# Kernel optimization log

Measured on AMD Instinct MI355X. Metric: run time of the kernel, lower is better.

Reference implementation:

```python
import jax, jax.numpy as jnp
import numpy as np


def setup_inputs() -> dict:
    key = jax.random.key(0)
    ks = jax.random.split(key, 8)
    B, L, D = 8, 4096, 1024
    s = 1.0 / np.sqrt(D)  # torch Linear default init scale (approx)
    return {
        "x": jax.random.normal(ks[0], (B, L, D), dtype=jnp.float32),
        "hidden": jax.random.normal(ks[1], (B, D), dtype=jnp.float32),
        "W_f": jax.random.normal(ks[2], (D, D), dtype=jnp.float32) * s,
        "b_f": jnp.zeros((D,), dtype=jnp.float32),
        "W_i": jax.random.normal(ks[3], (D, D), dtype=jnp.float32) * s,
        "b_i": jnp.zeros((D,), dtype=jnp.float32),
        "W_o": jax.random.normal(ks[4], (D, D), dtype=jnp.float32) * s,
        "b_o": jnp.zeros((D,), dtype=jnp.float32),
    }


def reference(x, hidden, W_f, b_f, W_i, b_i, W_o, b_o):
    # x: [B, L, D], hidden: [B, D]
    D = x.shape[-1]
    lin = jnp.linspace(0.0, 1.0, D, dtype=x.dtype)  # per-channel gate scale
    remember = jax.nn.sigmoid(jnp.einsum('bld,ed->ble', x, W_f) + b_f) * lin
    forget = 1.0 - remember
    inp = jnp.tanh(jnp.einsum('bld,ed->ble', x, W_i) + b_i) * remember

    # linear recurrence h_t = forget_t * h_{t-1} + inp_t  via parallel scan
    def combine(c1, c2):
        a1, u1 = c1
        a2, u2 = c2
        return (a1 * a2, a2 * u1 + u2)

    cumprod_forget, h_inner = jax.lax.associative_scan(combine, (forget, inp), axis=1)
    h = h_inner + hidden[:, None, :] * cumprod_forget  # inject initial hidden state
    y = jnp.einsum('bld,ed->ble', h, W_o) + b_o
    return y, h
```

## Files before the change

kernel.cpp:

```cpp
#include <hip/hip_runtime.h>
#include <stdint.h>

#define B_ 8
#define L_ 4096
#define D_ 1024
#define M_ (B_*L_)
#define CHUNKS 128
#define TCH (L_/CHUNKS)

typedef float f32x4 __attribute__((ext_vector_type(4)));
typedef float f32x2 __attribute__((ext_vector_type(2)));
typedef short short8 __attribute__((ext_vector_type(8)));
typedef unsigned short ushort4v __attribute__((ext_vector_type(4)));

static __device__ __forceinline__ unsigned short f2bf(float f) {
  union { float f; unsigned u; } v; v.f = f;
  unsigned r = v.u + 0x7FFFu + ((v.u >> 16) & 1u);
  return (unsigned short)(r >> 16);
}
static __device__ __forceinline__ float bf2f(unsigned short u) {
  union { unsigned u; float f; } v; v.u = ((unsigned)u) << 16; return v.f;
}

#define GLOAD16(g, l) \
  __builtin_amdgcn_global_load_lds((__attribute__((address_space(1))) const void*)(g), \
                                   (__attribute__((address_space(3))) void*)(l), 16, 0, 0)

__global__ __launch_bounds__(256)
void cvt_bf16(const float* __restrict__ src, unsigned short* __restrict__ dst, int n8)
{
  int gid = blockIdx.x * 256 + threadIdx.x;
  if (gid >= n8) return;
  const f32x4* s = (const f32x4*)(src + (size_t)gid * 8);
  f32x4 v0 = s[0], v1 = s[1];
  union { short8 v; unsigned short u[8]; } w;
  w.u[0] = f2bf(v0[0]); w.u[1] = f2bf(v0[1]); w.u[2] = f2bf(v0[2]); w.u[3] = f2bf(v0[3]);
  w.u[4] = f2bf(v1[0]); w.u[5] = f2bf(v1[1]); w.u[6] = f2bf(v1[2]); w.u[7] = f2bf(v1[3]);
  *(short8*)(dst + (size_t)gid * 8) = w.v;
}

__global__ __launch_bounds__(256)
void cvt_w3(const float* __restrict__ w0, const float* __restrict__ w1,
            const float* __restrict__ w2, unsigned short* __restrict__ dst)
{
  const int per = (D_ * D_) / 8 / 256;
  int m = blockIdx.x / per;
  int gid = (blockIdx.x % per) * 256 + threadIdx.x;
  const float* src = (m == 0) ? w0 : (m == 1) ? w1 : w2;
  const f32x4* s = (const f32x4*)(src + (size_t)gid * 8);
  f32x4 v0 = s[0], v1 = s[1];
  union { short8 v; unsigned short u[8]; } w;
  w.u[0] = f2bf(v0[0]); w.u[1] = f2bf(v0[1]); w.u[2] = f2bf(v0[2]); w.u[3] = f2bf(v0[3]);
  w.u[4] = f2bf(v1[0]); w.u[5] = f2bf(v1[1]); w.u[6] = f2bf(v1[2]); w.u[7] = f2bf(v1[3]);
  *(short8*)(dst + (size_t)m * D_ * D_ + (size_t)gid * 8) = w.v;
}

template<int MODE>
__global__ __launch_bounds__(512, 2)
void gemm256(const unsigned short* __restrict__ A,
             const unsigned short* __restrict__ Bw,
             const float* __restrict__ bias0,
             const float* __restrict__ bias1,
             unsigned short* __restrict__ ob0,
             unsigned short* __restrict__ ob1,
             float* __restrict__ of)
{
  __shared__ unsigned short lds[65536];
  char* ldsb = (char*)lds;

  const int tid  = threadIdx.x;
  const int lane = tid & 63;
  const int wid  = tid >> 6;
  const int wm   = wid >> 2;
  const int wn   = wid & 3;
  const int frow = lane & 15, ks = lane >> 4;
  const int xsw  = (ks ^ ((frow >> 1) & 3)) << 4;

  constexpr int NBN = (MODE == 0) ? 8 : 4;
  constexpr int GBM = 32 / NBN;
  const int xcd   = blockIdx.x & 7;
  const int slot  = blockIdx.x >> 3;
  const int local = slot & 31;
  const int wrnd  = slot >> 5;
  const int bm = (xcd * 16 + wrnd * GBM + (local & (GBM - 1))) * 256;
  const int bn = (local / GBM) * 256;

  const int r0  = tid >> 2;
  const int scl = ((tid & 3) ^ ((r0 >> 1) & 3)) << 4;
  const char* pA = (const char*)A  + (size_t)(bm + r0) * 2048 + scl;
  const char* pB = (const char*)Bw + (size_t)(bn + r0) * 2048 + scl;
  const int dst16 = tid * 16;

  f32x4 acc[8][4] = {};
  short8 aq[4], bq[4];

  auto stgA = [&](int T, int kk, int buf) {
    const char* s = pA + T * 128 + kk * 64;
    char* d = ldsb + buf * 32768 + kk * 16384 + dst16;
    GLOAD16(s, d);
    GLOAD16(s + (size_t)128 * 2048, d + 8192);
  };
  auto stgB = [&](int T, int kk, int buf) {
    const char* s = pB + T * 128 + kk * 64;
    char* d = ldsb + 65536 + buf * 32768 + kk * 16384 + dst16;
    GLOAD16(s, d);
    GLOAD16(s + (size_t)128 * 2048, d + 8192);
  };
  auto ldAB4 = [&](const char* LA, const char* LB, int kk, int ih) {
    const char* ab = LA + kk * 16384 + (wm * 128 + ih * 64 + frow) * 64 + xsw;
    const char* bb = LB + kk * 16384 + (wn * 64 + frow) * 64 + xsw;
    aq[0] = *(const short8*)(ab);
    bq[0] = *(const short8*)(bb);
    bq[1] = *(const short8*)(bb + 1024);
    bq[2] = *(const short8*)(bb + 2048);
    bq[3] = *(const short8*)(bb + 3072);
    aq[1] = *(const short8*)(ab + 1024);
    aq[2] = *(const short8*)(ab + 2048);
    aq[3] = *(const short8*)(ab + 3072);
  };
  auto ldA4 = [&](const char* LA, int kk, int ih) {
    const char* ab = LA + kk * 16384 + (wm * 128 + ih * 64 + frow) * 64 + xsw;
    aq[0] = *(const short8*)(ab);
    aq[1] = *(const short8*)(ab + 1024);
    aq[2] = *(const short8*)(ab + 2048);
    aq[3] = *(const short8*)(ab + 3072);
  };
  auto mfma16 = [&](int ih) {
    __builtin_amdgcn_s_setprio(1);
    #pragma unroll
    for (int i2 = 0; i2 < 4; ++i2) {
      #pragma unroll
      for (int j = 0; j < 4; ++j)
        acc[ih * 4 + i2][j] =
          __builtin_amdgcn_mfma_f32_16x16x32_bf16(aq[i2], bq[j], acc[ih * 4 + i2][j], 0, 0, 0);
    }
    __builtin_amdgcn_s_setprio(0);
  };

#define DO_TILE(T, BUF, STG1, STG2, W1, W3)                                   \
  {                                                                           \
    const char* LA = ldsb + (BUF) * 32768;                                    \
    const char* LB = ldsb + 65536 + (BUF) * 32768;                            \
    ldAB4(LA, LB, 0, 0);                                                      \
    if (STG1) stgA((T) + 1, 1, ((T) + 1) & 1);                                \
    __builtin_amdgcn_s_barrier();                                             \
    mfma16(0);                                                                \
    __builtin_amdgcn_s_barrier();                                             \
    ldA4(LA, 0, 1);                                                           \
    if (STG1) stgB((T) + 1, 1, ((T) + 1) & 1);                                \
    asm volatile("s_waitcnt vmcnt(" #W1 ")" ::: "memory");                    \
    __builtin_amdgcn_s_barrier();                                             \
    mfma16(1);                                                                \
    __builtin_amdgcn_s_barrier();                                             \
    ldAB4(LA, LB, 1, 0);                                                      \
    if (STG2) stgA((T) + 2, 0, (BUF));                                        \
    __builtin_amdgcn_s_barrier();                                             \
    mfma16(0);                                                                \
    __builtin_amdgcn_s_barrier();                                             \
    ldA4(LA, 1, 1);                                                           \
    if (STG2) stgB((T) + 2, 0, (BUF));                                        \
    asm volatile("s_waitcnt vmcnt(" #W3 ")" ::: "memory");                    \
    __builtin_amdgcn_s_barrier();                                             \
    mfma16(1);                                                                \
    __builtin_amdgcn_s_barrier();                                             \
  }

  stgA(0, 0, 0); stgB(0, 0, 0);
  stgA(0, 1, 0); stgB(0, 1, 0);
  stgA(1, 0, 1); stgB(1, 0, 1);
  asm volatile("s_waitcnt vmcnt(8)" ::: "memory");
  __builtin_amdgcn_s_barrier();

  for (int tt = 0; tt < 7; ++tt) {
    int t0 = tt * 2;
    DO_TILE(t0,     0, true, true, 8, 8);
    DO_TILE(t0 + 1, 1, true, true, 8, 8);
  }
  DO_TILE(14, 0, true,  false, 8, 4);
  DO_TILE(15, 1, false, false, 0, 0);
#undef DO_TILE

  if constexpr (MODE == 0) {
    const int plane = bn >> 10;
    const int cb    = bn & 1023;
    unsigned short* ob = plane ? ob1 : ob0;
    const float* bs    = plane ? bias1 : bias0;
    float bv[4];
    #pragma unroll
    for (int j = 0; j < 4; ++j) bv[j] = bs[cb + wn * 64 + j * 16 + frow];
    #pragma unroll
    for (int ii = 0; ii < 8; ++ii) {
      int row = bm + wm * 128 + ii * 16 + ks * 4;
      #pragma unroll
      for (int j = 0; j < 4; ++j) {
        int col = cb + wn * 64 + j * 16 + frow;
        float lin = (float)col * (1.0f / 1023.0f);
        #pragma unroll
        for (int r = 0; r < 4; ++r) {
          float z = acc[ii][j][r] + bv[j];
          float v;
          if (plane == 0) {
            v = lin / (1.0f + __expf(-z));
          } else {
            float e2 = __expf(2.0f * z);
            v = 1.0f - 2.0f / (e2 + 1.0f);
          }
          ob[(size_t)(row + r) * D_ + col] = f2bf(v);
        }
      }
    }
  } else {
    float bv[4];
    #pragma unroll
    for (int j = 0; j < 4; ++j) bv[j] = bias0[bn + wn * 64 + j * 16 + frow];
    #pragma unroll
    for (int ii = 0; ii < 8; ++ii) {
      int row = bm + wm * 128 + ii * 16 + ks * 4;
      #pragma unroll
      for (int j = 0; j < 4; ++j) {
        int col = bn + wn * 64 + j * 16 + frow;
        #pragma unroll
        for (int r = 0; r < 4; ++r)
          of[(size_t)(row + r) * D_ + col] = acc[ii][j][r] + bv[j];
      }
    }
  }
}

__global__ __launch_bounds__(256)
void scan_partial_b(const unsigned short* __restrict__ rb,
                    const unsigned short* __restrict__ tb,
                    float* __restrict__ Ag, float* __restrict__ Ug)
{
  int blk = blockIdx.x;
  int b = blk >> 7, c = blk & (CHUNKS - 1);
  int e = threadIdx.x << 2;
  size_t base = ((size_t)b * L_ + (size_t)c * TCH) * D_ + e;
  f32x4 a = {1.f,1.f,1.f,1.f}, u = {0.f,0.f,0.f,0.f};
  for (int t = 0; t < TCH; ++t) {
    ushort4v r4 = *(const ushort4v*)(rb + base + (size_t)t * D_);
    ushort4v t4 = *(const ushort4v*)(tb + base + (size_t)t * D_);
    #pragma unroll
    for (int j = 0; j < 4; ++j) {
      float rem = bf2f(r4[j]);
      float f   = 1.0f - rem;
      float inp = bf2f(t4[j]) * rem;
      u[j] = fmaf(f, u[j], inp);
      a[j] *= f;
    }
  }
  size_t o = (size_t)(b * CHUNKS + c) * D_ + e;
  *(f32x4*)(Ag + o) = a;
  *(f32x4*)(Ug + o) = u;
}

__global__ __launch_bounds__(256)
void scan_carry(const float* __restrict__ Ag, const float* __restrict__ Ug,
                const float* __restrict__ hidden, float* __restrict__ Hin)
{
  int gid = blockIdx.x * 256 + threadIdx.x;
  int b = gid >> 8;
  int e = (gid & 255) << 2;
  f32x4 h = *(const f32x4*)(hidden + (size_t)b * D_ + e);
  for (int c = 0; c < CHUNKS; ++c) {
    size_t o = (size_t)(b * CHUNKS + c) * D_ + e;
    *(f32x4*)(Hin + o) = h;
    f32x4 A = *(const f32x4*)(Ag + o);
    f32x4 U = *(const f32x4*)(Ug + o);
    h = A * h + U;
  }
}

__global__ __launch_bounds__(256)
void scan_apply_b(const unsigned short* __restrict__ rb,
                  const unsigned short* __restrict__ tb,
                  const float* __restrict__ Hin,
                  float* __restrict__ hout, unsigned short* __restrict__ hb)
{
  int blk = blockIdx.x;
  int b = blk >> 7, c = blk & (CHUNKS - 1);
  int e = threadIdx.x << 2;
  size_t base = ((size_t)b * L_ + (size_t)c * TCH) * D_ + e;
  f32x4 h = *(const f32x4*)(Hin + (size_t)(b * CHUNKS + c) * D_ + e);
  for (int t = 0; t < TCH; ++t) {
    size_t o = base + (size_t)t * D_;
    ushort4v r4 = *(const ushort4v*)(rb + o);
    ushort4v t4 = *(const ushort4v*)(tb + o);
    #pragma unroll
    for (int j = 0; j < 4; ++j) {
      float rem = bf2f(r4[j]);
      float f   = 1.0f - rem;
      float inp = bf2f(t4[j]) * rem;
      h[j] = fmaf(f, h[j], inp);
    }
    *(f32x4*)(hout + o) = h;
    ushort4v p;
    p[0] = f2bf(h[0]); p[1] = f2bf(h[1]); p[2] = f2bf(h[2]); p[3] = f2bf(h[3]);
    *(ushort4v*)(hb + o) = p;
  }
}

template<int MODE>
__global__ __launch_bounds__(256, 2)
void gemm_slow(const float* __restrict__ A, const float* __restrict__ B0,
               const float* __restrict__ B1, const float* __restrict__ bias0,
               const float* __restrict__ bias1, float* __restrict__ out0,
               float* __restrict__ out1)
{
  constexpr int BK = 32;
  __shared__ unsigned short As[128 * BK];
  __shared__ unsigned short Bs0[128 * BK];
  __shared__ unsigned short Bs1[(MODE == 0) ? (128 * BK) : 8];

  const int tid = threadIdx.x, lane = tid & 63, wave = tid >> 6;
  const int wr = wave >> 1, wc = wave & 1;
  const int bm = blockIdx.x * 128, bn = blockIdx.y * 128;
  f32x4 acc0[4][4] = {};
  f32x4 acc1[(MODE == 0) ? 4 : 1][(MODE == 0) ? 4 : 1] = {};
  const int frow = lane & 15, kslot = lane >> 4;
  const int xs = kslot ^ (frow & 3);

  auto stage = [&](const float* src, unsigned short* dst) {
    #pragma unroll
    for (int p = 0; p < 4; ++p) {
      int g = p * 256 + tid;
      int row = g >> 3, kq = (g & 7) << 2;
      f32x4 v = *(const f32x4*)(src + (size_t)row * D_ + kq);
      ushort4v w;
      w[0] = f2bf(v[0]); w[1] = f2bf(v[1]); w[2] = f2bf(v[2]); w[3] = f2bf(v[3]);
      int byte = kq << 1, slot = byte >> 4, sub = byte & 15;
      int off = row * 64 + ((slot ^ (row & 3)) << 4) + sub;
      *(ushort4v*)((char*)dst + off) = w;
    }
  };

  for (int k0 = 0; k0 < D_; k0 += BK) {
    stage(A + (size_t)bm * D_ + k0, As);
    stage(B0 + (size_t)bn * D_ + k0, Bs0);
    if constexpr (MODE == 0) stage(B1 + (size_t)bn * D_ + k0, Bs1);
    __syncthreads();
    short8 af[4], bf0[4], bf1[4];
    #pragma unroll
    for (int i = 0; i < 4; ++i) {
      int ar = wr * 64 + i * 16 + frow;
      af[i] = *(const short8*)((const char*)As + ar * 64 + (xs << 4));
      int br = wc * 64 + i * 16 + frow;
      bf0[i] = *(const short8*)((const char*)Bs0 + br * 64 + (xs << 4));
      if constexpr (MODE == 0)
        bf1[i] = *(const short8*)((const char*)Bs1 + br * 64 + (xs << 4));
    }
    #pragma unroll
    for (int i = 0; i < 4; ++i)
      #pragma unroll
      for (int j = 0; j < 4; ++j) {
        acc0[i][j] = __builtin_amdgcn_mfma_f32_16x16x32_bf16(af[i], bf0[j], acc0[i][j], 0, 0, 0);
        if constexpr (MODE == 0)
          acc1[i][j] = __builtin_amdgcn_mfma_f32_16x16x32_bf16(af[i], bf1[j], acc1[i][j], 0, 0, 0);
      }
    __syncthreads();
  }
  #pragma unroll
  for (int i = 0; i < 4; ++i)
    #pragma unroll
    for (int j = 0; j < 4; ++j)
      #pragma unroll
      for (int r = 0; r < 4; ++r) {
        int row = bm + wr * 64 + i * 16 + (lane >> 4) * 4 + r;
        int col = bn + wc * 64 + j * 16 + (lane & 15);
        size_t idx = (size_t)row * D_ + col;
        if constexpr (MODE == 0) {
          float zf = acc0[i][j][r] + bias0[col];
          float linv = (float)col * (1.0f / 1023.0f);
          float rem = linv / (1.0f + __expf(-zf));
          float zi = acc1[i][j][r] + bias1[col];
          float e2 = __expf(2.0f * zi);
          float th = 1.0f - 2.0f / (e2 + 1.0f);
          out0[idx] = 1.0f - rem;
          out1[idx] = th * rem;
        } else {
          out0[idx] = acc0[i][j][r] + bias0[col];
        }
      }
}

__global__ __launch_bounds__(256)
void scan_partial_f(const float* __restrict__ p0, const float* __restrict__ p1,
                    float* __restrict__ Ag, float* __restrict__ Ug)
{
  int blk = blockIdx.x;
  int b = blk / (CHUNKS * 2);
  int c = (blk >> 1) & (CHUNKS - 1);
  int e = ((blk & 1) << 9) + threadIdx.x * 2;
  size_t base = ((size_t)b * L_ + (size_t)c * TCH) * D_ + e;
  f32x2 a = {1.0f, 1.0f}, u = {0.0f, 0.0f};
  for (int t = 0; t < TCH; ++t) {
    f32x2 f = *(const f32x2*)(p0 + base + (size_t)t * D_);
    f32x2 i = *(const f32x2*)(p1 + base + (size_t)t * D_);
    u = f * u + i;
    a = a * f;
  }
  size_t o = (size_t)(b * CHUNKS + c) * D_ + e;
  *(f32x2*)(Ag + o) = a;
  *(f32x2*)(Ug + o) = u;
}

__global__ __launch_bounds__(256)
void scan_apply_f(const float* __restrict__ p0, float* __restrict__ p1_io,
                  const float* __restrict__ Hin)
{
  int blk = blockIdx.x;
  int b = blk / (CHUNKS * 2);
  int c = (blk >> 1) & (CHUNKS - 1);
  int e = ((blk & 1) << 9) + threadIdx.x * 2;
  size_t base = ((size_t)b * L_ + (size_t)c * TCH) * D_ + e;
  f32x2 h = *(const f32x2*)(Hin + (size_t)(b * CHUNKS + c) * D_ + e);
  for (int t = 0; t < TCH; ++t) {
    size_t o = base + (size_t)t * D_;
    f32x2 f = *(const f32x2*)(p0 + o);
    f32x2 i = *(const f32x2*)(p1_io + o);
    h = f * h + i;
    *(f32x2*)(p1_io + o) = h;
  }
}

extern "C" void kernel_launch(void* const* d_in, const int* in_sizes, int n_in,
                              void* d_out, int out_size, void* d_ws, size_t ws_size,
                              hipStream_t stream)
{
  const float* x      = (const float*)d_in[0];
  const float* hidden = (const float*)d_in[1];
  const float* W_f    = (const float*)d_in[2];
  const float* b_f    = (const float*)d_in[3];
  const float* W_i    = (const float*)d_in[4];
  const float* b_i    = (const float*)d_in[5];
  const float* W_o    = (const float*)d_in[6];
  const float* b_o    = (const float*)d_in[7];

  float* y = (float*)d_out;
  float* h = y + (size_t)M_ * D_;

  const size_t xb_elems = (size_t)M_ * D_;
  const size_t w_elems  = (size_t)D_ * D_;
  const size_t agg      = (size_t)B_ * CHUNKS * D_;
  const size_t need = (xb_elems * 3 + 3 * w_elems) * 2 + agg * 3 * 4;

  if (ws_size >= need) {
    unsigned short* xb  = (unsigned short*)d_ws;
    unsigned short* wfb = xb + xb_elems;
    unsigned short* wib = wfb + w_elems;
    unsigned short* wob = wib + w_elems;
    unsigned short* rbv = wob + w_elems;
    unsigned short* tbv = rbv + xb_elems;
    float* Ag  = (float*)(tbv + xb_elems);
    float* Ug  = Ag + agg;
    float* Hin = Ug + agg;

    cvt_bf16<<<(int)(xb_elems / 8 / 256), 256, 0, stream>>>(x, xb, (int)(xb_elems / 8));
    cvt_w3<<<3 * (int)(w_elems / 8 / 256), 256, 0, stream>>>(W_f, W_i, W_o, wfb);

    gemm256<0><<<1024, 512, 0, stream>>>(xb, wfb, b_f, b_i, rbv, tbv, nullptr);

    int pblocks = B_ * CHUNKS;
    scan_partial_b<<<pblocks, 256, 0, stream>>>(rbv, tbv, Ag, Ug);
    scan_carry<<<(B_ * D_ / 4) / 256, 256, 0, stream>>>(Ag, Ug, hidden, Hin);
    scan_apply_b<<<pblocks, 256, 0, stream>>>(rbv, tbv, Hin, h, xb);

    gemm256<1><<<512, 512, 0, stream>>>(xb, wob, b_o, nullptr, nullptr, nullptr, y);
  } else {
    float* Ag  = (float*)d_ws;
    float* Ug  = Ag + agg;
    float* Hin = Ug + agg;
    dim3 gg(M_ / 128, D_ / 128);
    int pblocks = B_ * CHUNKS * 2;

    gemm_slow<0><<<gg, 256, 0, stream>>>(x, W_f, W_i, b_f, b_i, y, h);
    scan_partial_f<<<pblocks, 256, 0, stream>>>(y, h, Ag, Ug);
    scan_carry<<<(B_ * D_ / 4) / 256, 256, 0, stream>>>(Ag, Ug, hidden, Hin);
    scan_apply_f<<<pblocks, 256, 0, stream>>>(y, h, Hin);
    gemm_slow<1><<<gg, 256, 0, stream>>>(h, W_o, nullptr, b_o, nullptr, y, nullptr);
  }
}
```

Baseline: 388.7 us.

## Triple-buffer A tiles in LDS and restructure GEMM prefetch schedule

```diff
diff --git a/kernel.cpp b/kernel.cpp
--- a/kernel.cpp
+++ b/kernel.cpp
@@ -65,7 +65,7 @@
              unsigned short* __restrict__ ob1,
              float* __restrict__ of)
 {
-  __shared__ unsigned short lds[65536];
+  __shared__ unsigned short lds[81920];
   char* ldsb = (char*)lds;
 
   const int tid  = threadIdx.x;
@@ -94,20 +94,24 @@
   f32x4 acc[8][4] = {};
   short8 aq[4], bq[4];
 
-  auto stgA = [&](int T, int kk, int buf) {
-    const char* s = pA + T * 128 + kk * 64;
-    char* d = ldsb + buf * 32768 + kk * 16384 + dst16;
-    GLOAD16(s, d);
+  auto stgA = [&](int T, int sl) {
+    const char* s = pA + T * 128;
+    char* d = ldsb + sl * 32768 + dst16;
+    GLOAD16(s,                      d);
     GLOAD16(s + (size_t)128 * 2048, d + 8192);
-  };
-  auto stgB = [&](int T, int kk, int buf) {
-    const char* s = pB + T * 128 + kk * 64;
-    char* d = ldsb + 65536 + buf * 32768 + kk * 16384 + dst16;
-    GLOAD16(s, d);
+    GLOAD16(s + 64,                      d + 16384);
+    GLOAD16(s + 64 + (size_t)128 * 2048, d + 24576);
+  };
+  auto stgB = [&](int T, int sl) {
+    const char* s = pB + T * 128;
+    char* d = ldsb + 98304 + sl * 32768 + dst16;
+    GLOAD16(s,                      d);
     GLOAD16(s + (size_t)128 * 2048, d + 8192);
-  };
-  auto ldAB4 = [&](const char* LA, const char* LB, int kk, int ih) {
-    const char* ab = LA + kk * 16384 + (wm * 128 + ih * 64 + frow) * 64 + xsw;
+    GLOAD16(s + 64,                      d + 16384);
+    GLOAD16(s + 64 + (size_t)128 * 2048, d + 24576);
+  };
+  auto ldAB4 = [&](const char* LA, const char* LB, int kk) {
+    const char* ab = LA + kk * 16384 + (wm * 128 + frow) * 64 + xsw;
     const char* bb = LB + kk * 16384 + (wn * 64 + frow) * 64 + xsw;
     aq[0] = *(const short8*)(ab);
     bq[0] = *(const short8*)(bb);
@@ -118,8 +122,8 @@
     aq[2] = *(const short8*)(ab + 2048);
     aq[3] = *(const short8*)(ab + 3072);
   };
-  auto ldA4 = [&](const char* LA, int kk, int ih) {
-    const char* ab = LA + kk * 16384 + (wm * 128 + ih * 64 + frow) * 64 + xsw;
+  auto ldA4 = [&](const char* LA, int kk) {
+    const char* ab = LA + kk * 16384 + (wm * 128 + 64 + frow) * 64 + xsw;
     aq[0] = *(const short8*)(ab);
     aq[1] = *(const short8*)(ab + 1024);
     aq[2] = *(const short8*)(ab + 2048);
@@ -137,48 +141,51 @@
     __builtin_amdgcn_s_setprio(0);
   };
 
-#define DO_TILE(T, BUF, STG1, STG2, W1, W3)                                   \
+#define BAR __builtin_amdgcn_s_barrier()
+#define DO_TILE(T, SA, SB, SAst, SBst, STGB, STGA, WAITN)                     \
   {                                                                           \
-    const char* LA = ldsb + (BUF) * 32768;                                    \
-    const char* LB = ldsb + 65536 + (BUF) * 32768;                            \
-    ldAB4(LA, LB, 0, 0);                                                      \
-    if (STG1) stgA((T) + 1, 1, ((T) + 1) & 1);                                \
-    __builtin_amdgcn_s_barrier();                                             \
-    mfma16(0);                                                                \
-    __builtin_amdgcn_s_barrier();                                             \
-    ldA4(LA, 0, 1);                                                           \
-    if (STG1) stgB((T) + 1, 1, ((T) + 1) & 1);                                \
-    asm volatile("s_waitcnt vmcnt(" #W1 ")" ::: "memory");                    \
-    __builtin_amdgcn_s_barrier();                                             \
-    mfma16(1);                                                                \
-    __builtin_amdgcn_s_barrier();                                             \
-    ldAB4(LA, LB, 1, 0);                                                      \
-    if (STG2) stgA((T) + 2, 0, (BUF));                                        \
-    __builtin_amdgcn_s_barrier();                                             \
-    mfma16(0);                                                                \
-    __builtin_amdgcn_s_barrier();                                             \
-    ldA4(LA, 1, 1);                                                           \
-    if (STG2) stgB((T) + 2, 0, (BUF));                                        \
-    asm volatile("s_waitcnt vmcnt(" #W3 ")" ::: "memory");                    \
-    __builtin_amdgcn_s_barrier();                                             \
-    mfma16(1);                                                                \
-    __builtin_amdgcn_s_barrier();                                             \
-  }
-
-  stgA(0, 0, 0); stgB(0, 0, 0);
-  stgA(0, 1, 0); stgB(0, 1, 0);
-  stgA(1, 0, 1); stgB(1, 0, 1);
+    const char* LA = ldsb + (SA) * 32768;                                     \
+    const char* LB = ldsb + 98304 + (SB) * 32768;                             \
+    ldAB4(LA, LB, 0);                                                         \
+    if (STGB) stgB((T) + 1, (SBst));                                          \
+    if (STGA) stgA((T) + 2, (SAst));                                          \
+    BAR; mfma16(0); BAR;                                                      \
+    ldA4(LA, 0);                                                              \
+    BAR; mfma16(1); BAR;                                                      \
+    ldAB4(LA, LB, 1);                                                         \
+    BAR; mfma16(0); BAR;                                                      \
+    ldA4(LA, 1);                                                              \
+    BAR; mfma16(1);                                                           \
+    if ((WAITN) >= 0) {                                                       \
+      if ((WAITN) == 4) asm volatile("s_waitcnt vmcnt(4)" ::: "memory");      \
+      else              asm volatile("s_waitcnt vmcnt(0)" ::: "memory");      \
+    }                                                                         \
+    BAR;                                                                      \
+  }
+
+  stgB(0, 0); stgA(0, 0);
+  stgB(1, 1); stgA(1, 1);
   asm volatile("s_waitcnt vmcnt(8)" ::: "memory");
-  __builtin_amdgcn_s_barrier();
-
-  for (int tt = 0; tt < 7; ++tt) {
-    int t0 = tt * 2;
-    DO_TILE(t0,     0, true, true, 8, 8);
-    DO_TILE(t0 + 1, 1, true, true, 8, 8);
-  }
-  DO_TILE(14, 0, true,  false, 8, 4);
-  DO_TILE(15, 1, false, false, 0, 0);
+  BAR;
+
+  DO_TILE( 0, 0, 0, 2, 1, false, true,  4);
+  DO_TILE( 1, 1, 1, 0, 0, true,  true,  4);
+  DO_TILE( 2, 2, 0, 1, 1, true,  true,  4);
+  DO_TILE( 3, 0, 1, 2, 0, true,  true,  4);
+  DO_TILE( 4, 1, 0, 0, 1, true,  true,  4);
+  DO_TILE( 5, 2, 1, 1, 0, true,  true,  4);
+  DO_TILE( 6, 0, 0, 2, 1, true,  true,  4);
+  DO_TILE( 7, 1, 1, 0, 0, true,  true,  4);
+  DO_TILE( 8, 2, 0, 1, 1, true,  true,  4);
+  DO_TILE( 9, 0, 1, 2, 0, true,  true,  4);
+  DO_TILE(10, 1, 0, 0, 1, true,  true,  4);
+  DO_TILE(11, 2, 1, 1, 0, true,  true,  4);
+  DO_TILE(12, 0, 0, 2, 1, true,  true,  4);
+  DO_TILE(13, 1, 1, 0, 0, true,  true,  4);
+  DO_TILE(14, 2, 0, 1, 1, true,  false, 0);
+  DO_TILE(15, 0, 1, 0, 0, false, false, -1);
 #undef DO_TILE
+#undef BAR
 
   if constexpr (MODE == 0) {
     const int plane = bn >> 10;
```

Result: slower. 411.9 us (+6.0%).

## Replace double-buffered GEMM mainloop with 5-slot ring and single barrier per chunk

Applied to the files above, without the earlier changes.

```diff
diff --git a/kernel.cpp b/kernel.cpp
--- a/kernel.cpp
+++ b/kernel.cpp
@@ -65,7 +65,7 @@
              unsigned short* __restrict__ ob1,
              float* __restrict__ of)
 {
-  __shared__ unsigned short lds[65536];
+  __shared__ unsigned short lds[81920];
   char* ldsb = (char*)lds;
 
   const int tid  = threadIdx.x;
@@ -94,21 +94,21 @@
   f32x4 acc[8][4] = {};
   short8 aq[4], bq[4];
 
-  auto stgA = [&](int T, int kk, int buf) {
-    const char* s = pA + T * 128 + kk * 64;
-    char* d = ldsb + buf * 32768 + kk * 16384 + dst16;
-    GLOAD16(s, d);
+  auto stgA = [&](int c, int sl) {
+    const char* s = pA + c * 64;
+    char* d = ldsb + sl * 16384 + dst16;
+    GLOAD16(s,                      d);
     GLOAD16(s + (size_t)128 * 2048, d + 8192);
   };
-  auto stgB = [&](int T, int kk, int buf) {
-    const char* s = pB + T * 128 + kk * 64;
-    char* d = ldsb + 65536 + buf * 32768 + kk * 16384 + dst16;
-    GLOAD16(s, d);
+  auto stgB = [&](int c, int sl) {
+    const char* s = pB + c * 64;
+    char* d = ldsb + 81920 + sl * 16384 + dst16;
+    GLOAD16(s,                      d);
     GLOAD16(s + (size_t)128 * 2048, d + 8192);
   };
-  auto ldAB4 = [&](const char* LA, const char* LB, int kk, int ih) {
-    const char* ab = LA + kk * 16384 + (wm * 128 + ih * 64 + frow) * 64 + xsw;
-    const char* bb = LB + kk * 16384 + (wn * 64 + frow) * 64 + xsw;
+  auto ldAB4 = [&](const char* LA, const char* LB) {
+    const char* ab = LA + (wm * 128 + frow) * 64 + xsw;
+    const char* bb = LB + (wn * 64 + frow) * 64 + xsw;
     aq[0] = *(const short8*)(ab);
     bq[0] = *(const short8*)(bb);
     bq[1] = *(const short8*)(bb + 1024);
@@ -118,8 +118,8 @@
     aq[2] = *(const short8*)(ab + 2048);
     aq[3] = *(const short8*)(ab + 3072);
   };
-  auto ldA4 = [&](const char* LA, int kk, int ih) {
-    const char* ab = LA + kk * 16384 + (wm * 128 + ih * 64 + frow) * 64 + xsw;
+  auto ldA4 = [&](const char* LA) {
+    const char* ab = LA + (wm * 128 + 64 + frow) * 64 + xsw;
     aq[0] = *(const short8*)(ab);
     aq[1] = *(const short8*)(ab + 1024);
     aq[2] = *(const short8*)(ab + 2048);
@@ -137,48 +137,74 @@
     __builtin_amdgcn_s_setprio(0);
   };
 
-#define DO_TILE(T, BUF, STG1, STG2, W1, W3)                                   \
+#define BAR __builtin_amdgcn_s_barrier()
+#define WAITV(N) asm volatile("s_waitcnt vmcnt(" #N ")" ::: "memory")
+#define DO_CH(c, SL, SG, STG, WN)                                             \
   {                                                                           \
-    const char* LA = ldsb + (BUF) * 32768;                                    \
-    const char* LB = ldsb + 65536 + (BUF) * 32768;                            \
-    ldAB4(LA, LB, 0, 0);                                                      \
-    if (STG1) stgA((T) + 1, 1, ((T) + 1) & 1);                                \
-    __builtin_amdgcn_s_barrier();                                             \
+    const char* LA = ldsb + (SL) * 16384;                                     \
+    const char* LB = ldsb + 81920 + (SL) * 16384;                             \
+    ldAB4(LA, LB);                                                            \
+    if (STG) stgA((c) + 4, (SG));                                             \
     mfma16(0);                                                                \
-    __builtin_amdgcn_s_barrier();                                             \
-    ldA4(LA, 0, 1);                                                           \
-    if (STG1) stgB((T) + 1, 1, ((T) + 1) & 1);                                \
-    asm volatile("s_waitcnt vmcnt(" #W1 ")" ::: "memory");                    \
-    __builtin_amdgcn_s_barrier();                                             \
+    ldA4(LA);                                                                 \
+    if (STG) stgB((c) + 4, (SG));                                             \
     mfma16(1);                                                                \
-    __builtin_amdgcn_s_barrier();                                             \
-    ldAB4(LA, LB, 1, 0);                                                      \
-    if (STG2) stgA((T) + 2, 0, (BUF));                                        \
-    __builtin_amdgcn_s_barrier();                                             \
+    WAITV(WN);                                                                \
+    BAR;                                                                      \
+  }
+#define DO_CH_LAST(SL)                                                        \
+  {                                                                           \
+    const char* LA = ldsb + (SL) * 16384;                                     \
+    const char* LB = ldsb + 81920 + (SL) * 16384;                             \
+    ldAB4(LA, LB);                                                            \
     mfma16(0);                                                                \
-    __builtin_amdgcn_s_barrier();                                             \
-    ldA4(LA, 1, 1);                                                           \
-    if (STG2) stgB((T) + 2, 0, (BUF));                                        \
-    asm volatile("s_waitcnt vmcnt(" #W3 ")" ::: "memory");                    \
-    __builtin_amdgcn_s_barrier();                                             \
+    ldA4(LA);                                                                 \
     mfma16(1);                                                                \
-    __builtin_amdgcn_s_barrier();                                             \
-  }
-
-  stgA(0, 0, 0); stgB(0, 0, 0);
-  stgA(0, 1, 0); stgB(0, 1, 0);
-  stgA(1, 0, 1); stgB(1, 0, 1);
-  asm volatile("s_waitcnt vmcnt(8)" ::: "memory");
-  __builtin_amdgcn_s_barrier();
-
-  for (int tt = 0; tt < 7; ++tt) {
-    int t0 = tt * 2;
-    DO_TILE(t0,     0, true, true, 8, 8);
-    DO_TILE(t0 + 1, 1, true, true, 8, 8);
-  }
-  DO_TILE(14, 0, true,  false, 8, 4);
-  DO_TILE(15, 1, false, false, 0, 0);
-#undef DO_TILE
+  }
+
+  stgA(0, 0); stgB(0, 0);
+  stgA(1, 1); stgB(1, 1);
+  stgA(2, 2); stgB(2, 2);
+  stgA(3, 3); stgB(3, 3);
+  WAITV(12);
+  BAR;
+
+  DO_CH( 0, 0, 4, true, 12);
+  DO_CH( 1, 1, 0, true, 12);
+  DO_CH( 2, 2, 1, true, 12);
+  DO_CH( 3, 3, 2, true, 12);
+  DO_CH( 4, 4, 3, true, 12);
+  DO_CH( 5, 0, 4, true, 12);
+  DO_CH( 6, 1, 0, true, 12);
+  DO_CH( 7, 2, 1, true, 12);
+  DO_CH( 8, 3, 2, true, 12);
+  DO_CH( 9, 4, 3, true, 12);
+  DO_CH(10, 0, 4, true, 12);
+  DO_CH(11, 1, 0, true, 12);
+  DO_CH(12, 2, 1, true, 12);
+  DO_CH(13, 3, 2, true, 12);
+  DO_CH(14, 4, 3, true, 12);
+  DO_CH(15, 0, 4, true, 12);
+  DO_CH(16, 1, 0, true, 12);
+  DO_CH(17, 2, 1, true, 12);
+  DO_CH(18, 3, 2, true, 12);
+  DO_CH(19, 4, 3, true, 12);
+  DO_CH(20, 0, 4, true, 12);
+  DO_CH(21, 1, 0, true, 12);
+  DO_CH(22, 2, 1, true, 12);
+  DO_CH(23, 3, 2, true, 12);
+  DO_CH(24, 4, 3, true, 12);
+  DO_CH(25, 0, 4, true, 12);
+  DO_CH(26, 1, 0, true, 12);
+  DO_CH(27, 2, 1, true, 12);
+  DO_CH(28, 3, 0, false, 8);
+  DO_CH(29, 4, 0, false, 4);
+  DO_CH(30, 0, 0, false, 0);
+  DO_CH_LAST(1);
+#undef DO_CH
+#undef DO_CH_LAST
+#undef WAITV
+#undef BAR
 
   if constexpr (MODE == 0) {
     const int plane = bn >> 10;
```

After: 386.6 us. No clear change (-0.5%).
